# Kernel tuning notes

Hardware: AMD Instinct MI355X
Metric: run time of the kernel (lower is better)

## Reference

```python
import jax, jax.numpy as jnp
import numpy as np

NUM_GRAPHS = 32

def leaky(x):
    return jax.nn.leaky_relu(x, 0.1)

def setup_inputs() -> dict:
    key = jax.random.key(0)
    ks = jax.random.split(key, 32)
    N, E = 8000, 32000
    x = jax.random.normal(ks[0], (N, 4), dtype=jnp.float32)
    edge_index = jax.random.randint(ks[1], (2, E), 0, N, dtype=jnp.int32)
    batch_index = jnp.sort(jax.random.randint(ks[2], (N,), 0, NUM_GRAPHS, dtype=jnp.int32))
    def lin(k, i, o, s=0.1):
        k1, k2 = jax.random.split(k)
        return jax.random.normal(k1, (i, o), dtype=jnp.float32) * s, jax.random.normal(k2, (o,), dtype=jnp.float32) * s
    p = {}
    # edge networks: Linear(3,64)+LeakyReLU+Linear(64, in*out)+LeakyReLU
    p['en1_w1'], p['en1_b1'] = lin(ks[3], 3, 64)
    p['en1_w2'], p['en1_b2'] = lin(ks[4], 64, 4 * 8)
    p['en2_w1'], p['en2_b1'] = lin(ks[5], 3, 64)
    p['en2_w2'], p['en2_b2'] = lin(ks[6], 64, 8 * 64)
    p['en3_w1'], p['en3_b1'] = lin(ks[7], 3, 64)
    p['en3_w2'], p['en3_b2'] = lin(ks[8], 64, 64 * 128)
    # NNConv root weights + biases
    p['root1'], p['cb1'] = lin(ks[9], 4, 8)
    p['root2'], p['cb2'] = lin(ks[10], 8, 64)
    p['root3'], p['cb3'] = lin(ks[11], 64, 128)
    # readout MLP
    p['fc1_w'], p['fc1_b'] = lin(ks[12], 128, 128)
    p['fc2_w'], p['fc2_b'] = lin(ks[13], 128, 64)
    p['fc3_w'], p['fc3_b'] = lin(ks[14], 64, 1)
    return dict(x=x, edge_index=edge_index, batch_index=batch_index, **p)

def nnconv(h, edge_index, edge_attr, w1, b1, w2, b2, root, cbias, in_ch, out_ch):
    # per-edge weight matrix from edge attributes
    e = leaky(edge_attr @ w1 + b1)              # [E,64]
    W = leaky(e @ w2 + b2).reshape(-1, in_ch, out_ch)  # [E,in,out]
    msg = jnp.einsum('ei,eio->eo', h[edge_index[0]], W)  # gather + per-edge matmul
    agg = jax.ops.segment_sum(msg, edge_index[1], num_segments=h.shape[0])  # scatter-add
    return agg + h @ root + cbias

def reference(x, edge_index, batch_index, en1_w1, en1_b1, en1_w2, en1_b2, en2_w1, en2_b1, en2_w2, en2_b2, en3_w1, en3_b1, en3_w2, en3_b2, root1, cb1, root2, cb2, root3, cb3, fc1_w, fc1_b, fc2_w, fc2_b, fc3_w, fc3_b):
    edge_attr = (x[edge_index[1]] - x[edge_index[0]])[:, 1:]  # [E,3] relative position
    h = leaky(nnconv(x, edge_index, edge_attr, en1_w1, en1_b1, en1_w2, en1_b2, root1, cb1, 4, 8))
    h = leaky(nnconv(h, edge_index, edge_attr, en2_w1, en2_b1, en2_w2, en2_b2, root2, cb2, 8, 64))
    h = leaky(nnconv(h, edge_index, edge_attr, en3_w1, en3_b1, en3_w2, en3_b2, root3, cb3, 64, 128))
    g = jax.ops.segment_sum(h, batch_index, num_segments=NUM_GRAPHS)  # sum-pool per graph
    g = leaky(g @ fc1_w + fc1_b)
    g = leaky(g @ fc2_w + fc2_b)
    return g @ fc3_w + fc3_b  # [G,1] total energies
```

## Files before the change

kernel.cpp:

```cpp
#include <hip/hip_runtime.h>
#include <hip/hip_bf16.h>

typedef __attribute__((ext_vector_type(8))) short short8;
typedef __attribute__((ext_vector_type(4))) float floatx4;
typedef __attribute__((ext_vector_type(2))) float float2v;

__device__ __forceinline__ float leaky(float v){ return v > 0.f ? v : 0.1f*v; }
__device__ __forceinline__ void atomAdd(float* p, float v){ unsafeAtomicAdd(p, v); }
__device__ __forceinline__ short f2bf(float f){
  __hip_bfloat16 h = __float2bfloat16(f);
  return *reinterpret_cast<short*>(&h);
}

struct P {
  const float *x; const int *ei; const int *batch;
  const float *en1_w1,*en1_b1,*en1_w2,*en1_b2;
  const float *en2_w1,*en2_b1,*en2_w2,*en2_b2;
  const float *en3_w1,*en3_b1,*en3_w2,*en3_b2;
  const float *root1,*cb1,*root2,*cb2,*root3,*cb3;
  const float *fc1w,*fc1b,*fc2w,*fc2b,*fc3w,*fc3b;
  short *ef2b,*ef3b,*w2p2,*w2p3;
  float *a1,*a2,*a3,*g,*out;
  int N,E,Epad;
};

__global__ __launch_bounds__(256) void fused0(P p){
  int bid = blockIdx.x, tid = threadIdx.x;
  int nEf = p.Epad/4;
  if (bid < nEf){
    __shared__ float sm[4][64];
    int id = bid*256 + tid;
    int e = id >> 6, j = id & 63;
    float v1 = 0.f;
    if (e >= p.E){
      p.ef2b[id] = 0; p.ef3b[id] = 0;
    } else {
      int s = p.ei[e], d = p.ei[p.E+e];
      float4 xs = *reinterpret_cast<const float4*>(p.x + (size_t)s*4);
      float4 xd = *reinterpret_cast<const float4*>(p.x + (size_t)d*4);
      float d0 = xd.y - xs.y, d1 = xd.z - xs.z, d2 = xd.w - xs.w;
      v1 = leaky(d0*p.en1_w1[j] + d1*p.en1_w1[64+j] + d2*p.en1_w1[128+j] + p.en1_b1[j]);
      p.ef2b[id] = f2bf(leaky(d0*p.en2_w1[j] + d1*p.en2_w1[64+j] + d2*p.en2_w1[128+j] + p.en2_b1[j]));
      p.ef3b[id] = f2bf(leaky(d0*p.en3_w1[j] + d1*p.en3_w1[64+j] + d2*p.en3_w1[128+j] + p.en3_b1[j]));
    }
    sm[tid >> 6][j] = v1;
    __syncthreads();
    if (tid < 32){
      int le = tid >> 3, o = tid & 7;
      int ge = bid*4 + le;
      if (ge < p.E){
        int s = p.ei[ge], d = p.ei[p.E+ge];
        float z[4];
        #pragma unroll
        for (int i=0;i<4;i++) z[i] = p.en1_b2[i*8+o];
        for (int k=0;k<64;k++){
          float a = sm[le][k];
          #pragma unroll
          for (int i=0;i<4;i++) z[i] += a*p.en1_w2[k*32 + i*8 + o];
        }
        float4 xv = *reinterpret_cast<const float4*>(p.x + (size_t)s*4);
        float msg = xv.x*leaky(z[0]) + xv.y*leaky(z[1]) + xv.z*leaky(z[2]) + xv.w*leaky(z[3]);
        atomAdd(&p.a1[(size_t)d*8 + o], msg);
      }
    }
  } else {
    int pb = bid - nEf;
    int lane = tid & 63;
    int c = pb*4 + (tid >> 6);
    const float* w2; short* dst; int ICOC, OT, cc;
    if (c < 64){ w2 = p.en2_w2; dst = p.w2p2; ICOC = 512;  OT = 4; cc = c; }
    else       { w2 = p.en3_w2; dst = p.w2p3; ICOC = 8192; OT = 8; cc = c - 64; }
    int kh = cc & 1, rem = cc >> 1, otg = rem % OT, i = rem / OT;
    int n = lane & 15, q = lane >> 4;
    short o8[8];
    #pragma unroll
    for (int j=0;j<8;j++){
      int k = kh*32 + q*8 + j;
      o8[j] = f2bf(w2[(size_t)k*ICOC + i*(OT*16) + otg*16 + n]);
    }
    *reinterpret_cast<short8*>(dst + (size_t)cc*512 + lane*8) = *reinterpret_cast<short8*>(o8);
  }
}

__global__ __launch_bounds__(256) void conv2k(P p){
  __shared__ float hsT[8][32];
  __shared__ int sdst[32];
  int tid = threadIdx.x;
  int eb = blockIdx.x*32;
  int E = p.E;
  {
    int e = tid & 31, i = tid >> 5;
    int ge = eb + e;
    bool valid = ge < E;
    int src = valid ? p.ei[ge] : 0;
    float hv = 0.f;
    if (valid){
      float4 xv = *reinterpret_cast<const float4*>(p.x + (size_t)src*4);
      float v = p.a1[(size_t)src*8 + i] + p.cb1[i]
              + xv.x*p.root1[i] + xv.y*p.root1[8+i] + xv.z*p.root1[16+i] + xv.w*p.root1[24+i];
      hv = leaky(v);
    }
    hsT[i][e] = hv;
    if (tid < 32) sdst[tid] = (eb + tid < E) ? p.ei[E + eb + tid] : -1;
  }
  __syncthreads();

  int lane = tid & 63, wv = tid >> 6;
  int n = lane & 15, quad = lane >> 4;
  int o0 = wv*16;
  short8 A[2][2];
  #pragma unroll
  for (int m=0;m<2;m++)
    #pragma unroll
    for (int kh=0;kh<2;kh++)
      A[m][kh] = *reinterpret_cast<const short8*>(p.ef2b + (size_t)(eb + m*16 + n)*64 + kh*32 + quad*8);

  float2v msg[2][2];
  msg[0][0]=(float2v){0.f,0.f}; msg[0][1]=(float2v){0.f,0.f};
  msg[1][0]=(float2v){0.f,0.f}; msg[1][1]=(float2v){0.f,0.f};

  auto loadB = [&](int ii, short8 (&Bt)[2], float &bz){
    int ig = (ii < 8) ? ii : 7;
    #pragma unroll
    for (int kh=0;kh<2;kh++)
      Bt[kh] = *reinterpret_cast<const short8*>(p.w2p2 + ((size_t)((ig*4 + wv)*2 + kh) << 9) + lane*8);
    bz = p.en2_b2[ig*64 + o0 + n];
  };
  auto compute = [&](int ii, short8 (&Bt)[2], float bz){
    #pragma unroll
    for (int m=0;m<2;m++){
      float4 hv = *reinterpret_cast<const float4*>(&hsT[ii][m*16 + quad*4]);
      float2v hvl = {hv.x, hv.y}, hvh = {hv.z, hv.w};
      floatx4 z = {bz, bz, bz, bz};
      z = __builtin_amdgcn_mfma_f32_16x16x32_bf16(A[m][0], Bt[0], z, 0, 0, 0);
      z = __builtin_amdgcn_mfma_f32_16x16x32_bf16(A[m][1], Bt[1], z, 0, 0, 0);
      float2v zl = {z[0], z[1]}, zh = {z[2], z[3]};
      float2v ll = __builtin_elementwise_max(zl, zl*0.1f);
      float2v lh = __builtin_elementwise_max(zh, zh*0.1f);
      msg[m][0] += hvl*ll;
      msg[m][1] += hvh*lh;
    }
  };

  short8 B0[2], B1[2]; float bz0, bz1;
  loadB(0, B0, bz0);
  #pragma unroll 2
  for (int i=0;i<8;i+=2){
    loadB(i+1, B1, bz1);
    compute(i, B0, bz0);
    loadB(i+2, B0, bz0);
    compute(i+1, B1, bz1);
  }

  #pragma unroll
  for (int m=0;m<2;m++)
    #pragma unroll
    for (int r=0;r<4;r++){
      int d = sdst[m*16 + quad*4 + r];
      if (d >= 0) atomAdd(&p.a2[(size_t)d*64 + o0 + n], msg[m][r>>1][r&1]);
    }
}

__global__ __launch_bounds__(256) void conv3k(P p){
  __shared__ float hsT[32][64];
  __shared__ int sdst[64];
  __shared__ float r2s[512];
  __shared__ float cb2s[64];
  int tid = threadIdx.x;
  int bi = blockIdx.x;
  int eb = (bi >> 1)*64;
  int i0 = (bi & 1)*32;
  int E = p.E;

  r2s[tid]     = p.root2[tid];
  r2s[256+tid] = p.root2[256+tid];
  if (tid < 64) cb2s[tid] = p.cb2[tid];
  if (tid < 64) sdst[tid] = (eb + tid < E) ? p.ei[E + eb + tid] : -1;

  int e = tid & 63, c = tid >> 6;
  int ge = eb + e;
  bool valid = ge < E;
  int src = valid ? p.ei[ge] : 0;
  float h1[8];
  {
    float4 xv  = *reinterpret_cast<const float4*>(p.x  + (size_t)src*4);
    float4 a1l = *reinterpret_cast<const float4*>(p.a1 + (size_t)src*8);
    float4 a1h = *reinterpret_cast<const float4*>(p.a1 + (size_t)src*8 + 4);
    float a1v[8] = {a1l.x,a1l.y,a1l.z,a1l.w,a1h.x,a1h.y,a1h.z,a1h.w};
    #pragma unroll
    for (int k=0;k<8;k++){
      float v = a1v[k] + p.cb1[k] + xv.x*p.root1[k] + xv.y*p.root1[8+k]
              + xv.z*p.root1[16+k] + xv.w*p.root1[24+k];
      h1[k] = leaky(v);
    }
  }
  __syncthreads();
  {
    int ib = i0 + c*8;
    float4 acc0 = *reinterpret_cast<const float4*>(p.a2 + (size_t)src*64 + ib);
    float4 acc1 = *reinterpret_cast<const float4*>(p.a2 + (size_t)src*64 + ib + 4);
    float4 cb0 = *reinterpret_cast<const float4*>(&cb2s[ib]);
    float4 cb1v = *reinterpret_cast<const float4*>(&cb2s[ib+4]);
    acc0.x+=cb0.x; acc0.y+=cb0.y; acc0.z+=cb0.z; acc0.w+=cb0.w;
    acc1.x+=cb1v.x; acc1.y+=cb1v.y; acc1.z+=cb1v.z; acc1.w+=cb1v.w;
    #pragma unroll
    for (int k=0;k<8;k++){
      float hk = h1[k];
      float4 r0 = *reinterpret_cast<const float4*>(&r2s[k*64+ib]);
      float4 r1 = *reinterpret_cast<const float4*>(&r2s[k*64+ib+4]);
      acc0.x += hk*r0.x; acc0.y += hk*r0.y; acc0.z += hk*r0.z; acc0.w += hk*r0.w;
      acc1.x += hk*r1.x; acc1.y += hk*r1.y; acc1.z += hk*r1.z; acc1.w += hk*r1.w;
    }
    hsT[c*8+0][e] = valid ? leaky(acc0.x) : 0.f;
    hsT[c*8+1][e] = valid ? leaky(acc0.y) : 0.f;
    hsT[c*8+2][e] = valid ? leaky(acc0.z) : 0.f;
    hsT[c*8+3][e] = valid ? leaky(acc0.w) : 0.f;
    hsT[c*8+4][e] = valid ? leaky(acc1.x) : 0.f;
    hsT[c*8+5][e] = valid ? leaky(acc1.y) : 0.f;
    hsT[c*8+6][e] = valid ? leaky(acc1.z) : 0.f;
    hsT[c*8+7][e] = valid ? leaky(acc1.w) : 0.f;
  }
  __syncthreads();

  int lane = tid & 63, wv = tid >> 6;
  int n = lane & 15, quad = lane >> 4;
  int o0 = wv*32;
  short8 A[4][2];
  #pragma unroll
  for (int m=0;m<4;m++)
    #pragma unroll
    for (int kh=0;kh<2;kh++)
      A[m][kh] = *reinterpret_cast<const short8*>(p.ef3b + (size_t)(eb + m*16 + n)*64 + kh*32 + quad*8);

  float2v msg[4][2][2];
  #pragma unroll
  for (int m=0;m<4;m++)
    #pragma unroll
    for (int t=0;t<2;t++){
      msg[m][t][0]=(float2v){0.f,0.f}; msg[m][t][1]=(float2v){0.f,0.f};
    }

  auto loadB = [&](int ii, short8 (&Bt)[2][2], float (&bzt)[2]){
    int il = (ii < 32) ? ii : 31;
    int ig = i0 + il;
    #pragma unroll
    for (int t=0;t<2;t++){
      int otg = wv*2 + t;
      #pragma unroll
      for (int kh=0;kh<2;kh++)
        Bt[t][kh] = *reinterpret_cast<const short8*>(p.w2p3 + ((size_t)((ig*8 + otg)*2 + kh) << 9) + lane*8);
      bzt[t] = p.en3_b2[ig*128 + o0 + t*16 + n];
    }
  };
  auto compute = [&](int ii, short8 (&Bt)[2][2], float (&bzt)[2]){
    #pragma unroll
    for (int m=0;m<4;m++){
      float4 hv = *reinterpret_cast<const float4*>(&hsT[ii][m*16 + quad*4]);
      float2v hvl = {hv.x, hv.y}, hvh = {hv.z, hv.w};
      #pragma unroll
      for (int t=0;t<2;t++){
        floatx4 z = {bzt[t], bzt[t], bzt[t], bzt[t]};
        z = __builtin_amdgcn_mfma_f32_16x16x32_bf16(A[m][0], Bt[t][0], z, 0, 0, 0);
        z = __builtin_amdgcn_mfma_f32_16x16x32_bf16(A[m][1], Bt[t][1], z, 0, 0, 0);
        float2v zl = {z[0], z[1]}, zh = {z[2], z[3]};
        float2v ll = __builtin_elementwise_max(zl, zl*0.1f);
        float2v lh = __builtin_elementwise_max(zh, zh*0.1f);
        msg[m][t][0] += hvl*ll;
        msg[m][t][1] += hvh*lh;
      }
    }
  };

  short8 B0[2][2], B1[2][2];
  float bz0[2], bz1[2];
  loadB(0, B0, bz0);
  #pragma unroll 2
  for (int i=0;i<32;i+=2){
    loadB(i+1, B1, bz1);
    compute(i, B0, bz0);
    loadB(i+2, B0, bz0);
    compute(i+1, B1, bz1);
  }

  #pragma unroll
  for (int m=0;m<4;m++)
    #pragma unroll
    for (int r=0;r<4;r++){
      int d = sdst[m*16 + quad*4 + r];
      if (d >= 0){
        #pragma unroll
        for (int t=0;t<2;t++)
          atomAdd(&p.a3[(size_t)d*128 + o0 + t*16 + n], msg[m][t][r>>1][r&1]);
      }
    }
}

__global__ __launch_bounds__(256) void npk(P p){
  __shared__ float r3s[8192];
  __shared__ float r2s[512];
  __shared__ float cb2s[64];
  __shared__ float hrow[16][64];
  int tid = threadIdx.x;
  int N = p.N;
  for (int r=tid; r<2048; r+=256)
    reinterpret_cast<float4*>(r3s)[r] = reinterpret_cast<const float4*>(p.root3)[r];
  r2s[tid]     = p.root2[tid];
  r2s[256+tid] = p.root2[256+tid];
  if (tid < 64) cb2s[tid] = p.cb2[tid];
  __syncthreads();

  int n0 = blockIdx.x*16;
  {
    int nl = tid >> 4, c0 = (tid & 15)*4;
    int n = n0 + nl;
    int nn = (n < N) ? n : 0;
    float4 xv  = *reinterpret_cast<const float4*>(p.x  + (size_t)nn*4);
    float4 a1l = *reinterpret_cast<const float4*>(p.a1 + (size_t)nn*8);
    float4 a1h = *reinterpret_cast<const float4*>(p.a1 + (size_t)nn*8 + 4);
    float a1v[8] = {a1l.x,a1l.y,a1l.z,a1l.w,a1h.x,a1h.y,a1h.z,a1h.w};
    float h1[8];
    #pragma unroll
    for (int k=0;k<8;k++){
      float v = a1v[k] + p.cb1[k] + xv.x*p.root1[k] + xv.y*p.root1[8+k]
              + xv.z*p.root1[16+k] + xv.w*p.root1[24+k];
      h1[k] = leaky(v);
    }
    float4 acc = *reinterpret_cast<const float4*>(p.a2 + (size_t)nn*64 + c0);
    float4 cbv = *reinterpret_cast<const float4*>(&cb2s[c0]);
    acc.x+=cbv.x; acc.y+=cbv.y; acc.z+=cbv.z; acc.w+=cbv.w;
    #pragma unroll
    for (int k=0;k<8;k++){
      float hk = h1[k];
      float4 rv = *reinterpret_cast<const float4*>(&r2s[k*64+c0]);
      acc.x += hk*rv.x; acc.y += hk*rv.y; acc.z += hk*rv.z; acc.w += hk*rv.w;
    }
    hrow[nl][c0+0] = leaky(acc.x);
    hrow[nl][c0+1] = leaky(acc.y);
    hrow[nl][c0+2] = leaky(acc.z);
    hrow[nl][c0+3] = leaky(acc.w);
  }
  __syncthreads();

  int o = tid & 127, np_ = tid >> 7;
  float acc = 0.f; int cur = -1;
  for (int rep=0; rep<8; rep++){
    int nl = rep*2 + np_; int n = n0 + nl;
    if (n >= N) break;
    int b = p.batch[n];
    if (b != cur){ if (cur >= 0) atomAdd(&p.g[cur*128+o], acc); acc = 0.f; cur = b; }
    float v = p.a3[(size_t)n*128 + o] + p.cb3[o];
    #pragma unroll 16
    for (int i=0;i<64;i++) v += hrow[nl][i]*r3s[i*128+o];
    acc += leaky(v);
  }
  if (cur >= 0) atomAdd(&p.g[cur*128+o], acc);
}

__global__ void head_kernel(P p){
  __shared__ float s1[128], s2[128];
  int gi = blockIdx.x, t = threadIdx.x;
  s1[t] = p.g[gi*128+t];
  __syncthreads();
  float v = p.fc1b[t];
  for (int i=0;i<128;i++) v += s1[i]*p.fc1w[i*128+t];
  s2[t] = leaky(v);
  __syncthreads();
  if (t < 64){
    float v2 = p.fc2b[t];
    for (int i=0;i<128;i++) v2 += s2[i]*p.fc2w[i*64+t];
    s1[t] = leaky(v2);
  }
  __syncthreads();
  if (t == 0){
    float v3 = p.fc3b[0];
    for (int i=0;i<64;i++) v3 += s1[i]*p.fc3w[i];
    p.out[gi] = v3;
  }
}

extern "C" void kernel_launch(void* const* d_in, const int* in_sizes, int n_in,
                              void* d_out, int out_size, void* d_ws, size_t ws_size,
                              hipStream_t stream) {
  P p;
  p.x      = (const float*)d_in[0];
  p.ei     = (const int*)  d_in[1];
  p.batch  = (const int*)  d_in[2];
  p.en1_w1 = (const float*)d_in[3];  p.en1_b1 = (const float*)d_in[4];
  p.en1_w2 = (const float*)d_in[5];  p.en1_b2 = (const float*)d_in[6];
  p.en2_w1 = (const float*)d_in[7];  p.en2_b1 = (const float*)d_in[8];
  p.en2_w2 = (const float*)d_in[9];  p.en2_b2 = (const float*)d_in[10];
  p.en3_w1 = (const float*)d_in[11]; p.en3_b1 = (const float*)d_in[12];
  p.en3_w2 = (const float*)d_in[13]; p.en3_b2 = (const float*)d_in[14];
  p.root1  = (const float*)d_in[15]; p.cb1    = (const float*)d_in[16];
  p.root2  = (const float*)d_in[17]; p.cb2    = (const float*)d_in[18];
  p.root3  = (const float*)d_in[19]; p.cb3    = (const float*)d_in[20];
  p.fc1w   = (const float*)d_in[21]; p.fc1b   = (const float*)d_in[22];
  p.fc2w   = (const float*)d_in[23]; p.fc2b   = (const float*)d_in[24];
  p.fc3w   = (const float*)d_in[25]; p.fc3b   = (const float*)d_in[26];
  p.out = (float*)d_out;

  p.N = in_sizes[0] / 4;
  p.E = in_sizes[1] / 2;
  p.Epad = (p.E + 63) & ~63;

  p.ef2b = (short*)d_ws;
  p.ef3b = p.ef2b + (size_t)p.Epad*64;
  p.w2p2 = p.ef3b + (size_t)p.Epad*64;
  p.w2p3 = p.w2p2 + 8*4*2*512;
  p.a1   = (float*)(p.w2p3 + 64*8*2*512);
  p.a2   = p.a1 + (size_t)p.N*8;
  p.a3   = p.a2 + (size_t)p.N*64;
  p.g    = p.a3 + (size_t)p.N*128;

  size_t zero_bytes = ((size_t)p.N*(8+64+128) + (size_t)32*128) * sizeof(float);
  hipMemsetAsync(p.a1, 0, zero_bytes, stream);

  fused0<<<p.Epad/4 + 272, 256, 0, stream>>>(p);
  conv2k<<<p.Epad/32, 256, 0, stream>>>(p);
  conv3k<<<(p.Epad/64)*2, 256, 0, stream>>>(p);
  npk<<<(p.N + 15)/16, 256, 0, stream>>>(p);
  head_kernel<<<32, 128, 0, stream>>>(p);
}
```

Before: 244.5 us.

## Parallelize layer-1 edge MLP across all threads, split conv3 launch, shrink npk tiles

In the layer-1 edge stage, the 64→32 second-layer matmul now runs on all four wavefronts with eight lanes each taking a k-slice, combined by xor shuffles, where before only 32 threads did the whole 64-step loop serially. conv3k gains a tile offset and is launched as two half-grids. npk processes 8 nodes per block instead of 16, doubling the block count. Each block still reloads the 32KB root3 matrix into shared memory, so halving the nodes per block doubles that load traffic. The split conv3 launch adds one extra kernel launch and has no obvious benefit.

```diff
diff --git a/kernel.cpp b/kernel.cpp
--- a/kernel.cpp
+++ b/kernel.cpp
@@ -45,22 +45,32 @@
     }
     sm[tid >> 6][j] = v1;
     __syncthreads();
-    if (tid < 32){
-      int le = tid >> 3, o = tid & 7;
-      int ge = bid*4 + le;
-      if (ge < p.E){
-        int s = p.ei[ge], d = p.ei[p.E+ge];
-        float z[4];
-        #pragma unroll
-        for (int i=0;i<4;i++) z[i] = p.en1_b2[i*8+o];
-        for (int k=0;k<64;k++){
-          float a = sm[le][k];
-          #pragma unroll
-          for (int i=0;i<4;i++) z[i] += a*p.en1_w2[k*32 + i*8 + o];
-        }
+    {
+      int wv = tid >> 6;
+      int lane = tid & 63;
+      int o = lane >> 3, kg = lane & 7;
+      int ge = bid*4 + wv;
+      float z0=0.f, z1=0.f, z2=0.f, z3=0.f;
+      const float* smw = &sm[wv][kg*8];
+      #pragma unroll
+      for (int kk=0;kk<8;kk++){
+        float a = smw[kk];
+        const float* wp = p.en1_w2 + (kg*8+kk)*32 + o;
+        z0 += a*wp[0]; z1 += a*wp[8]; z2 += a*wp[16]; z3 += a*wp[24];
+      }
+      #pragma unroll
+      for (int d=1; d<8; d<<=1){
+        z0 += __shfl_xor(z0, d);
+        z1 += __shfl_xor(z1, d);
+        z2 += __shfl_xor(z2, d);
+        z3 += __shfl_xor(z3, d);
+      }
+      if (kg == 0 && ge < p.E){
+        int s = p.ei[ge], dd = p.ei[p.E+ge];
+        z0 += p.en1_b2[o]; z1 += p.en1_b2[8+o]; z2 += p.en1_b2[16+o]; z3 += p.en1_b2[24+o];
         float4 xv = *reinterpret_cast<const float4*>(p.x + (size_t)s*4);
-        float msg = xv.x*leaky(z[0]) + xv.y*leaky(z[1]) + xv.z*leaky(z[2]) + xv.w*leaky(z[3]);
-        atomAdd(&p.a1[(size_t)d*8 + o], msg);
+        float msg = xv.x*leaky(z0) + xv.y*leaky(z1) + xv.z*leaky(z2) + xv.w*leaky(z3);
+        atomAdd(&p.a1[(size_t)dd*8 + o], msg);
       }
     }
   } else {
@@ -161,14 +171,14 @@
     }
 }
 
-__global__ __launch_bounds__(256) void conv3k(P p){
+__global__ __launch_bounds__(256) void conv3k(P p, int t0){
   __shared__ float hsT[32][64];
   __shared__ int sdst[64];
   __shared__ float r2s[512];
   __shared__ float cb2s[64];
   int tid = threadIdx.x;
   int bi = blockIdx.x;
-  int eb = (bi >> 1)*64;
+  int eb = ((bi >> 1) + t0)*64;
   int i0 = (bi & 1)*32;
   int E = p.E;
 
@@ -299,7 +309,7 @@
   __shared__ float r3s[8192];
   __shared__ float r2s[512];
   __shared__ float cb2s[64];
-  __shared__ float hrow[16][64];
+  __shared__ float hrow[8][64];
   int tid = threadIdx.x;
   int N = p.N;
   for (int r=tid; r<2048; r+=256)
@@ -309,9 +319,9 @@
   if (tid < 64) cb2s[tid] = p.cb2[tid];
   __syncthreads();
 
-  int n0 = blockIdx.x*16;
+  int n0 = blockIdx.x*8;
   {
-    int nl = tid >> 4, c0 = (tid & 15)*4;
+    int nl = tid >> 5, c0 = (tid & 31)*2;
     int n = n0 + nl;
     int nn = (n < N) ? n : 0;
     float4 xv  = *reinterpret_cast<const float4*>(p.x  + (size_t)nn*4);
@@ -325,25 +335,22 @@
               + xv.z*p.root1[16+k] + xv.w*p.root1[24+k];
       h1[k] = leaky(v);
     }
-    float4 acc = *reinterpret_cast<const float4*>(p.a2 + (size_t)nn*64 + c0);
-    float4 cbv = *reinterpret_cast<const float4*>(&cb2s[c0]);
-    acc.x+=cbv.x; acc.y+=cbv.y; acc.z+=cbv.z; acc.w+=cbv.w;
+    float2 acc = *reinterpret_cast<const float2*>(p.a2 + (size_t)nn*64 + c0);
+    acc.x += cb2s[c0]; acc.y += cb2s[c0+1];
     #pragma unroll
     for (int k=0;k<8;k++){
       float hk = h1[k];
-      float4 rv = *reinterpret_cast<const float4*>(&r2s[k*64+c0]);
-      acc.x += hk*rv.x; acc.y += hk*rv.y; acc.z += hk*rv.z; acc.w += hk*rv.w;
+      acc.x += hk*r2s[k*64+c0];
+      acc.y += hk*r2s[k*64+c0+1];
     }
     hrow[nl][c0+0] = leaky(acc.x);
     hrow[nl][c0+1] = leaky(acc.y);
-    hrow[nl][c0+2] = leaky(acc.z);
-    hrow[nl][c0+3] = leaky(acc.w);
   }
   __syncthreads();
 
   int o = tid & 127, np_ = tid >> 7;
   float acc = 0.f; int cur = -1;
-  for (int rep=0; rep<8; rep++){
+  for (int rep=0; rep<4; rep++){
     int nl = rep*2 + np_; int n = n0 + nl;
     if (n >= N) break;
     int b = p.batch[n];
@@ -417,7 +424,12 @@
 
   fused0<<<p.Epad/4 + 272, 256, 0, stream>>>(p);
   conv2k<<<p.Epad/32, 256, 0, stream>>>(p);
-  conv3k<<<(p.Epad/64)*2, 256, 0, stream>>>(p);
-  npk<<<(p.N + 15)/16, 256, 0, stream>>>(p);
+
+  int tiles = p.Epad/64;
+  int half = (tiles + 1)/2;
+  conv3k<<<half*2, 256, 0, stream>>>(p, 0);
+  conv3k<<<(tiles - half)*2, 256, 0, stream>>>(p, half);
+
+  npk<<<(p.N + 7)/8, 256, 0, stream>>>(p);
   head_kernel<<<32, 128, 0, stream>>>(p);
 }
```

Result: slower. 300.9 us (+23.1%).

## Batch 64 edges per block in fused0 with LDS-staged edge-net weights

Applied to the files above, without the earlier changes.

The edge-feature part of fused0 now handles 64 edges per block over 16 iterations instead of 4. It stages the first-layer weights and the en1 second-layer weights in shared memory once per block. The layer-1 message matmul now uses all 64 lanes per edge, splitting K in halves and reducing with shuffles, instead of only 32 threads doing serial 64-step loops. This targets the idle threads and repeated global weight reads in the old tail, at the cost of fewer blocks and an LDS staging prologue per block.

```diff
diff --git a/kernel.cpp b/kernel.cpp
--- a/kernel.cpp
+++ b/kernel.cpp
@@ -26,42 +26,66 @@
 
 __global__ __launch_bounds__(256) void fused0(P p){
   int bid = blockIdx.x, tid = threadIdx.x;
-  int nEf = p.Epad/4;
+  int nEf = p.Epad/64;
   if (bid < nEf){
+    __shared__ float w1s[3][192];
+    __shared__ float b1s[3][64];
+    __shared__ float w2s[2048];
+    __shared__ float b2s[32];
     __shared__ float sm[4][64];
-    int id = bid*256 + tid;
-    int e = id >> 6, j = id & 63;
-    float v1 = 0.f;
-    if (e >= p.E){
-      p.ef2b[id] = 0; p.ef3b[id] = 0;
-    } else {
-      int s = p.ei[e], d = p.ei[p.E+e];
+    for (int idx = tid; idx < 576; idx += 256){
+      int net = idx/192, r = idx%192;
+      w1s[net][r] = (net==0 ? p.en1_w1 : net==1 ? p.en2_w1 : p.en3_w1)[r];
+    }
+    if (tid < 192){
+      int net = tid >> 6, j = tid & 63;
+      b1s[net][j] = (net==0 ? p.en1_b1 : net==1 ? p.en2_b1 : p.en3_b1)[j];
+    }
+    for (int idx = tid; idx < 2048; idx += 256) w2s[idx] = p.en1_w2[idx];
+    if (tid < 32) b2s[tid] = p.en1_b2[tid];
+    __syncthreads();
+
+    int wv = tid >> 6, j = tid & 63;
+    int o = j & 31, h = j >> 5;
+    int e0 = bid*64;
+    for (int it = 0; it < 16; it++){
+      int e = e0 + it*4 + wv;
+      bool valid = e < p.E;
+      int s = valid ? p.ei[e] : 0;
+      int d = valid ? p.ei[p.E+e] : 0;
       float4 xs = *reinterpret_cast<const float4*>(p.x + (size_t)s*4);
       float4 xd = *reinterpret_cast<const float4*>(p.x + (size_t)d*4);
       float d0 = xd.y - xs.y, d1 = xd.z - xs.z, d2 = xd.w - xs.w;
-      v1 = leaky(d0*p.en1_w1[j] + d1*p.en1_w1[64+j] + d2*p.en1_w1[128+j] + p.en1_b1[j]);
-      p.ef2b[id] = f2bf(leaky(d0*p.en2_w1[j] + d1*p.en2_w1[64+j] + d2*p.en2_w1[128+j] + p.en2_b1[j]));
-      p.ef3b[id] = f2bf(leaky(d0*p.en3_w1[j] + d1*p.en3_w1[64+j] + d2*p.en3_w1[128+j] + p.en3_b1[j]));
-    }
-    sm[tid >> 6][j] = v1;
-    __syncthreads();
-    if (tid < 32){
-      int le = tid >> 3, o = tid & 7;
-      int ge = bid*4 + le;
-      if (ge < p.E){
-        int s = p.ei[ge], d = p.ei[p.E+ge];
-        float z[4];
-        #pragma unroll
-        for (int i=0;i<4;i++) z[i] = p.en1_b2[i*8+o];
-        for (int k=0;k<64;k++){
-          float a = sm[le][k];
-          #pragma unroll
-          for (int i=0;i<4;i++) z[i] += a*p.en1_w2[k*32 + i*8 + o];
-        }
-        float4 xv = *reinterpret_cast<const float4*>(p.x + (size_t)s*4);
-        float msg = xv.x*leaky(z[0]) + xv.y*leaky(z[1]) + xv.z*leaky(z[2]) + xv.w*leaky(z[3]);
-        atomAdd(&p.a1[(size_t)d*8 + o], msg);
+      float v1 = 0.f;
+      if (valid){
+        v1 = leaky(d0*w1s[0][j] + d1*w1s[0][64+j] + d2*w1s[0][128+j] + b1s[0][j]);
+        p.ef2b[(size_t)e*64+j] = f2bf(leaky(d0*w1s[1][j] + d1*w1s[1][64+j] + d2*w1s[1][128+j] + b1s[1][j]));
+        p.ef3b[(size_t)e*64+j] = f2bf(leaky(d0*w1s[2][j] + d1*w1s[2][64+j] + d2*w1s[2][128+j] + b1s[2][j]));
+      } else {
+        p.ef2b[(size_t)e*64+j] = 0;
+        p.ef3b[(size_t)e*64+j] = 0;
       }
+      sm[wv][j] = v1;
+
+      float za0=0.f, za1=0.f, za2=0.f, za3=0.f;
+      const float* smw = &sm[wv][h*32];
+      const float* wb = &w2s[(size_t)h*32*32 + o];
+      #pragma unroll
+      for (int k=0;k<32;k+=4){
+        za0 += smw[k+0]*wb[(k+0)*32];
+        za1 += smw[k+1]*wb[(k+1)*32];
+        za2 += smw[k+2]*wb[(k+2)*32];
+        za3 += smw[k+3]*wb[(k+3)*32];
+      }
+      float z = (za0+za1)+(za2+za3);
+      z += __shfl_xor(z, 32);
+      z = leaky(z + b2s[o]);
+      float xi = (o<16) ? ((o<8)? xs.x : xs.y) : ((o<24)? xs.z : xs.w);
+      float t = xi * z;
+      t += __shfl_xor(t, 8);
+      t += __shfl_xor(t, 16);
+      if (h == 0 && o < 8 && valid)
+        atomAdd(&p.a1[(size_t)d*8 + o], t);
     }
   } else {
     int pb = bid - nEf;
@@ -74,9 +98,9 @@
     int n = lane & 15, q = lane >> 4;
     short o8[8];
     #pragma unroll
-    for (int j=0;j<8;j++){
-      int k = kh*32 + q*8 + j;
-      o8[j] = f2bf(w2[(size_t)k*ICOC + i*(OT*16) + otg*16 + n]);
+    for (int jj=0;jj<8;jj++){
+      int k = kh*32 + q*8 + jj;
+      o8[jj] = f2bf(w2[(size_t)k*ICOC + i*(OT*16) + otg*16 + n]);
     }
     *reinterpret_cast<short8*>(dst + (size_t)cc*512 + lane*8) = *reinterpret_cast<short8*>(o8);
   }
@@ -415,7 +439,7 @@
   size_t zero_bytes = ((size_t)p.N*(8+64+128) + (size_t)32*128) * sizeof(float);
   hipMemsetAsync(p.a1, 0, zero_bytes, stream);
 
-  fused0<<<p.Epad/4 + 272, 256, 0, stream>>>(p);
+  fused0<<<p.Epad/64 + 272, 256, 0, stream>>>(p);
   conv2k<<<p.Epad/32, 256, 0, stream>>>(p);
   conv3k<<<(p.Epad/64)*2, 256, 0, stream>>>(p);
   npk<<<(p.N + 15)/16, 256, 0, stream>>>(p);
```

After: 248.1 us. Within noise of the previous version (+1.5%).
